# Optimization experiments

Measured on AMD Instinct MI355X. Metric: run time of the kernel, lower is better.

## Reference

```python
import jax, jax.numpy as jnp
import numpy as np

B, T, D, H, OUT_STEPS = 4096, 50, 64, 128, 100  # batch, warmup steps, latent dim, hidden units, rollout steps


def setup_inputs() -> dict:
    key = jax.random.key(0)
    ks = jax.random.split(key, 9)
    s = jnp.float32(0.05)  # keep gates out of saturation
    return {
        "x":   jax.random.normal(ks[0], (B, T, D), jnp.float32),
        "Wk0": jax.random.normal(ks[1], (D, 4 * H), jnp.float32) * s,
        "Wr0": jax.random.normal(ks[2], (H, 4 * H), jnp.float32) * s,
        "b0":  jax.random.normal(ks[3], (4 * H,), jnp.float32) * s,
        "Wk1": jax.random.normal(ks[4], (H, 4 * H), jnp.float32) * s,
        "Wr1": jax.random.normal(ks[5], (H, 4 * H), jnp.float32) * s,
        "b1":  jax.random.normal(ks[6], (4 * H,), jnp.float32) * s,
        "Wd":  jax.random.normal(ks[7], (H, D), jnp.float32) * s,
        "bd":  jax.random.normal(ks[8], (D,), jnp.float32) * s,
    }


def _lstm_cell(xt, h, c, Wk, Wr, b):
    # Keras LSTMCell: gates in order i, f, g(cell), o
    z = xt @ Wk + h @ Wr + b  # [B, 4H]
    i, f, g, o = jnp.split(z, 4, axis=-1)
    c_new = jax.nn.sigmoid(f) * c + jax.nn.sigmoid(i) * jnp.tanh(g)
    h_new = jax.nn.sigmoid(o) * jnp.tanh(c_new)
    return h_new, c_new


def reference(x, Wk0, Wr0, b0, Wk1, Wr1, b1, Wd, bd):
    Bn = x.shape[0]
    Hn = Wr0.shape[0]
    z = jnp.zeros((Bn, Hn), x.dtype)

    def warm_step(carry, xt):
        h0, c0, h1, c1 = carry
        h0, c0 = _lstm_cell(xt, h0, c0, Wk0, Wr0, b0)
        h1, c1 = _lstm_cell(h0, h1, c1, Wk1, Wr1, b1)
        return (h0, c0, h1, c1), None

    # warmup over the provided sequence (T >= min_warmup_steps=10)
    carry, _ = jax.lax.scan(warm_step, (z, z, z, z), jnp.swapaxes(x, 0, 1))
    pred0 = carry[2] @ Wd + bd  # Dense on last layer's hidden state

    def ar_step(carry, _):
        pred, h0, c0, h1, c1 = carry
        h0, c0 = _lstm_cell(pred, h0, c0, Wk0, Wr0, b0)
        h1, c1 = _lstm_cell(h0, h1, c1, Wk1, Wr1, b1)
        pred = h1 @ Wd + bd
        return (pred, h0, c0, h1, c1), pred

    _, preds = jax.lax.scan(ar_step, (pred0,) + carry, None, length=OUT_STEPS - 1)
    preds = jnp.concatenate([pred0[None], preds], axis=0)  # [OUT, B, D]
    return jnp.swapaxes(preds, 0, 1)  # [B, OUT, D]
```

## Files before the change

### kernel.cpp

```cpp
#include <hip/hip_runtime.h>
#include <hip/hip_bf16.h>

#define Tt   50
#define Dd   64
#define NOUT 100
#define G4   512
#define K0S  72
#define K1P  264
#define BM   16

typedef __attribute__((ext_vector_type(8))) short  short8;
typedef __attribute__((ext_vector_type(4))) float  floatx4;

#if __has_builtin(__builtin_amdgcn_exp2f)
#define EXP2(v) __builtin_amdgcn_exp2f(v)
#else
#define EXP2(v) exp2f(v)
#endif
__device__ __forceinline__ float rcp_(float v) { return __builtin_amdgcn_rcpf(v); }
#define KN2L2E (-2.8853900817779268f)

#define BARRIER() asm volatile("s_waitcnt lgkmcnt(0)\n\ts_barrier" ::: "memory")

__device__ __forceinline__ short f2bf(float f) {
    __hip_bfloat16 h = __float2bfloat16(f);
    return *reinterpret_cast<const short*>(&h);
}

#define W1F_OFF 196608
#define WDF_OFF 458752
#define B0F_OFF 475136
#define B1F_OFF 477184
#define BDF_OFF 479232

__global__ __launch_bounds__(256) void prep_kernel(
    const float* __restrict__ Wk0, const float* __restrict__ Wr0, const float* __restrict__ b0,
    const float* __restrict__ Wk1, const float* __restrict__ Wr1, const float* __restrict__ b1,
    const float* __restrict__ Wd,  const float* __restrict__ bd,  char* __restrict__ ws)
{
    int idx = blockIdx.x * 256 + threadIdx.x;
    short* w0f = (short*)ws;
    short* w1f = (short*)(ws + W1F_OFF);
    short* wdf = (short*)(ws + WDF_OFF);
    float* b0f = (float*)(ws + B0F_OFF);
    float* b1f = (float*)(ws + B1F_OFF);
    float* bdf = (float*)(ws + BDF_OFF);
    const float NL2E = -1.4426950408889634f;
    const float N2L2E = -2.8853900817779268f;

    if (idx < 98304) {
        int f = idx >> 9, r = idx & 511;
        int lane = r >> 3, j = r & 7;
        int nt = f / 6, kt = f - nt * 6;
        int k = kt * 32 + (lane >> 4) * 8 + j;
        int col = nt * 16 + (lane & 15);
        float sc = ((col >> 7) == 2) ? N2L2E : NL2E;
        w0f[idx] = f2bf(sc * ((k < Dd) ? Wk0[k * G4 + col] : Wr0[(k - Dd) * G4 + col]));
    } else if (idx < 229376) {
        int i2 = idx - 98304;
        int f = i2 >> 9, r = i2 & 511;
        int lane = r >> 3, j = r & 7;
        int nt = f >> 3, kt = f & 7;
        int k = kt * 32 + (lane >> 4) * 8 + j;
        int col = nt * 16 + (lane & 15);
        float sc = ((col >> 7) == 2) ? N2L2E : NL2E;
        w1f[i2] = f2bf(sc * ((k < 128) ? Wk1[k * G4 + col] : Wr1[(k - 128) * G4 + col]));
    } else if (idx < 237568) {
        int i2 = idx - 229376;
        int f = i2 >> 9, r = i2 & 511;
        int lane = r >> 3, j = r & 7;
        int nt = f >> 2, kt = f & 3;
        int k = kt * 32 + (lane >> 4) * 8 + j;
        int col = nt * 16 + (lane & 15);
        wdf[i2] = f2bf(Wd[k * Dd + col]);
    } else if (idx < 237568 + 1088) {
        int i2 = idx - 237568;
        if (i2 < 512) {
            float sc = ((i2 >> 7) == 2) ? N2L2E : NL2E;
            b0f[i2] = sc * b0[i2];
        } else if (i2 < 1024) {
            int c = i2 - 512;
            float sc = ((c >> 7) == 2) ? N2L2E : NL2E;
            b1f[c] = sc * b1[c];
        } else bdf[i2 - 1024] = bd[i2 - 1024];
    }
}

#define SM_A1  4608
#define SM_W0  21504
#define SM_TOT 152576
#define A0SZ   1152
#define A1SZ   4224

#define MFMA_B16(A, B, C) __builtin_amdgcn_mfma_f32_16x16x32_bf16((A), (B), (C), 0, 0, 0)

#define GATES(ACC, CS, BASE, COLOFF)                                                     \
    _Pragma("unroll")                                                                    \
    for (int rr = 0; rr < 4; ++rr) {                                                     \
        float Ei = EXP2(ACC[0][rr]);                                                     \
        float Ef = EXP2(ACC[1][rr]);                                                     \
        float Eg = EXP2(ACC[2][rr]);                                                     \
        float Eo = EXP2(ACC[3][rr]);                                                     \
        float ig = (1.0f - Eg) * rcp_((1.0f + Ei) * (1.0f + Eg));                        \
        float c_ = fmaf(rcp_(1.0f + Ef), CS[rr], ig);                                    \
        CS[rr] = c_;                                                                     \
        float Ec = EXP2(c_ * KN2L2E);                                                    \
        float h_ = (1.0f - Ec) * rcp_((1.0f + Eo) * (1.0f + Ec));                        \
        (BASE)[(quad * 4 + rr) * K1P + (COLOFF) + hu] = f2bf(h_);                        \
    }

#define ACC_INIT(ACC, B0_, B1_, B2_, B3_)            \
    ACC[0] = (floatx4){B0_, B0_, B0_, B0_};          \
    ACC[1] = (floatx4){B1_, B1_, B1_, B1_};          \
    ACC[2] = (floatx4){B2_, B2_, B2_, B2_};          \
    ACC[3] = (floatx4){B3_, B3_, B3_, B3_};

#define L0KT(KT)                                                                          \
    {                                                                                     \
        short8 af = ((KT) < 2)                                                            \
            ? *(const short8*)&a0p[l15 * K0S + (KT) * 32 + quad * 8]                      \
            : *(const short8*)&a1q[l15 * K1P + ((KT) - 2) * 32 + quad * 8];               \
        _Pragma("unroll")                                                                 \
        for (int g = 0; g < 4; ++g) {                                                     \
            const int pp = g * 6 + (KT);                                                  \
            short8 bfr = (pp < 16) ? *(const short8*)&w0l[((pp * 8 + w) << 9) + lane * 8] \
                                   : W0R[pp - 16];                                        \
            acc[g] = MFMA_B16(af, bfr, acc[g]);                                           \
        }                                                                                 \
    }

__global__ __launch_bounds__(512, 2) void lstm_kernel(
    const float* __restrict__ x, const char* __restrict__ ws, float* __restrict__ out)
{
    extern __shared__ char smem[];
    short* a0b = (short*)smem;
    short* a1b = (short*)(smem + SM_A1);
    short* w0l = (short*)(smem + SM_W0);

    const short* w0f = (const short*)ws;
    const short* w1f = (const short*)(ws + W1F_OFF);
    const short* wdf = (const short*)(ws + WDF_OFF);
    const float* b0f = (const float*)(ws + B0F_OFF);
    const float* b1f = (const float*)(ws + B1F_OFF);
    const float* bdf = (const float*)(ws + BDF_OFF);

    const int tid  = threadIdx.x;
    const int w    = tid >> 6;
    const int lane = tid & 63;
    const int l15  = lane & 15;
    const int quad = lane >> 4;
    const int row0 = blockIdx.x * BM;

    for (int i = tid; i < 2 * A0SZ; i += 512) a0b[i] = 0;
    for (int i = tid; i < 2 * A1SZ; i += 512) a1b[i] = 0;
    for (int c = tid; c < 8192; c += 512) {
        int e8 = c & 63;
        int wv = (c >> 6) & 7;
        int p  = c >> 9;
        int g = p / 6, kt = p - g * 6;
        const short* src = w0f + ((((g * 8 + wv) * 6) + kt) << 9) + e8 * 8;
        *(short8*)&w0l[((p * 8 + wv) << 9) + e8 * 8] = *(const short8*)src;
    }
    {
        int cx = tid & 63, rg2 = tid >> 6;
        a0b[rg2 * K0S + cx]       = f2bf(x[(size_t)(row0 + rg2) * (Tt * Dd) + cx]);
        a0b[(rg2 + 8) * K0S + cx] = f2bf(x[(size_t)(row0 + rg2 + 8) * (Tt * Dd) + cx]);
    }

    const short* w0rb = w0f + w * 3072 + lane * 8;
    const short* w1rb = w1f + w * 4096 + lane * 8;
    short8 W1R[4][8];
    #pragma unroll
    for (int g = 0; g < 4; ++g)
        #pragma unroll
        for (int kt = 0; kt < 8; ++kt)
            W1R[g][kt] = *(const short8*)(w1rb + g * 32768 + kt * 512);
    short8 W0R[8];
    #pragma unroll
    for (int p = 16; p < 24; ++p) {
        int g = p / 6, kt = p - g * 6;
        W0R[p - 16] = *(const short8*)(w0rb + g * 24576 + kt * 512);
    }
    short8 WdR[4];
    if (w < 4) {
        #pragma unroll
        for (int kt = 0; kt < 4; ++kt)
            WdR[kt] = *(const short8*)(wdf + ((w * 4 + kt) << 9) + lane * 8);
    }

    const int hu = w * 16 + l15;
    const float bi0 = b0f[hu], bff0 = b0f[128 + hu], bg0 = b0f[256 + hu], bo0 = b0f[384 + hu];
    const float bi1 = b1f[hu], bff1 = b1f[128 + hu], bg1 = b1f[256 + hu], bo1 = b1f[384 + hu];
    const float bdv = bdf[(w & 3) * 16 + l15];

    float c0s[4] = {0.f, 0.f, 0.f, 0.f};
    float c1s[4] = {0.f, 0.f, 0.f, 0.f};

    const int colx = tid & 63, rg = tid >> 6;

    __syncthreads();

    for (int step = 0; step < 149; ++step) {
        const int p = step & 1, q = p ^ 1;
        short* a0p = a0b + p * A0SZ;  short* a0q = a0b + q * A0SZ;
        short* a1p = a1b + p * A1SZ;  short* a1q = a1b + q * A1SZ;

        float xv0, xv1;
        if (step < Tt - 1) {
            xv0 = x[(size_t)(row0 + rg)     * (Tt * Dd) + (step + 1) * Dd + colx];
            xv1 = x[(size_t)(row0 + rg + 8) * (Tt * Dd) + (step + 1) * Dd + colx];
        }

        floatx4 acc[4];
        ACC_INIT(acc, bi0, bff0, bg0, bo0);
        __builtin_amdgcn_s_setprio(1);
        L0KT(2) L0KT(3) L0KT(4) L0KT(5) L0KT(0) L0KT(1)
        __builtin_amdgcn_s_setprio(0);

        GATES(acc, c0s, a1p, 0);

        if (step < Tt - 1) {
            a0q[rg * K0S + colx]       = f2bf(xv0);
            a0q[(rg + 8) * K0S + colx] = f2bf(xv1);
        }
        BARRIER();

        ACC_INIT(acc, bi1, bff1, bg1, bo1);
        __builtin_amdgcn_s_setprio(1);
        #pragma unroll
        for (int kt = 0; kt < 8; ++kt) {
            short8 af = *(const short8*)&a1p[l15 * K1P + kt * 32 + quad * 8];
            #pragma unroll
            for (int g = 0; g < 4; ++g)
                acc[g] = MFMA_B16(af, W1R[g][kt], acc[g]);
        }
        __builtin_amdgcn_s_setprio(0);

        GATES(acc, c1s, a1q, 128);

        if (step >= Tt - 1) {
            BARRIER();
            if (w < 4) {
                floatx4 ad0 = (floatx4){bdv, bdv, bdv, bdv};
                floatx4 ad1 = (floatx4){0.f, 0.f, 0.f, 0.f};
                __builtin_amdgcn_s_setprio(1);
                {
                    short8 a0_ = *(const short8*)&a1q[l15 * K1P + 128 +  0 + quad * 8];
                    short8 a1_ = *(const short8*)&a1q[l15 * K1P + 128 + 32 + quad * 8];
                    short8 a2_ = *(const short8*)&a1q[l15 * K1P + 128 + 64 + quad * 8];
                    short8 a3_ = *(const short8*)&a1q[l15 * K1P + 128 + 96 + quad * 8];
                    ad0 = MFMA_B16(a0_, WdR[0], ad0);
                    ad1 = MFMA_B16(a1_, WdR[1], ad1);
                    ad0 = MFMA_B16(a2_, WdR[2], ad0);
                    ad1 = MFMA_B16(a3_, WdR[3], ad1);
                }
                __builtin_amdgcn_s_setprio(0);
                float pv0 = ad0[0] + ad1[0], pv1 = ad0[1] + ad1[1];
                float pv2 = ad0[2] + ad1[2], pv3 = ad0[3] + ad1[3];
                int col = w * 16 + l15;
                a0q[(quad * 4 + 0) * K0S + col] = f2bf(pv0);
                a0q[(quad * 4 + 1) * K0S + col] = f2bf(pv1);
                a0q[(quad * 4 + 2) * K0S + col] = f2bf(pv2);
                a0q[(quad * 4 + 3) * K0S + col] = f2bf(pv3);
                int s = step - (Tt - 1);
                size_t ob = (size_t)(row0 + quad * 4) * (NOUT * Dd) + s * Dd + col;
                out[ob]                 = pv0;
                out[ob + 1 * NOUT * Dd] = pv1;
                out[ob + 2 * NOUT * Dd] = pv2;
                out[ob + 3 * NOUT * Dd] = pv3;
            }
            BARRIER();
        }
    }
}

extern "C" void kernel_launch(void* const* d_in, const int* in_sizes, int n_in,
                              void* d_out, int out_size, void* d_ws, size_t ws_size,
                              hipStream_t stream)
{
    (void)in_sizes; (void)n_in; (void)out_size; (void)ws_size;
    static_assert(SM_TOT <= 160 * 1024, "LDS budget");
    hipFuncSetAttribute(reinterpret_cast<const void*>(lstm_kernel),
                        hipFuncAttributeMaxDynamicSharedMemorySize, SM_TOT);
    prep_kernel<<<933, 256, 0, stream>>>(
        (const float*)d_in[1], (const float*)d_in[2], (const float*)d_in[3],
        (const float*)d_in[4], (const float*)d_in[5], (const float*)d_in[6],
        (const float*)d_in[7], (const float*)d_in[8], (char*)d_ws);
    lstm_kernel<<<256, 512, SM_TOT, stream>>>(
        (const float*)d_in[0], (const char*)d_ws, (float*)d_out);
}
```

Before: 468.6 us.

## Split warmup and rollout loops and overlap layer-1 recurrent MFMAs with barrier

Splits the single step loop into a warmup loop and an autoregressive loop, which removes the per-step branches on the step index. In the rollout loop, the layer-1 MFMAs over the h1 half of the input (k-tiles 4-7, written the previous step) are issued before the barrier. Only the k-tiles that depend on the freshly written h0 run after it. This shortens the critical path around the synchronisation in the sequential recurrence, in exchange for duplicated code and a larger instruction footprint.

```diff
diff --git a/kernel.cpp b/kernel.cpp
--- a/kernel.cpp
+++ b/kernel.cpp
@@ -129,6 +129,14 @@
         }                                                                                 \
     }
 
+#define L1KT(KT)                                                                          \
+    {                                                                                     \
+        short8 af = *(const short8*)&a1p[l15 * K1P + (KT) * 32 + quad * 8];               \
+        _Pragma("unroll")                                                                 \
+        for (int g = 0; g < 4; ++g)                                                       \
+            acc[g] = MFMA_B16(af, W1R[g][KT], acc[g]);                                    \
+    }
+
 __global__ __launch_bounds__(512, 2) void lstm_kernel(
     const float* __restrict__ x, const char* __restrict__ ws, float* __restrict__ out)
 {
@@ -200,16 +208,13 @@
 
     __syncthreads();
 
-    for (int step = 0; step < 149; ++step) {
+    for (int step = 0; step < 49; ++step) {
         const int p = step & 1, q = p ^ 1;
         short* a0p = a0b + p * A0SZ;  short* a0q = a0b + q * A0SZ;
         short* a1p = a1b + p * A1SZ;  short* a1q = a1b + q * A1SZ;
 
-        float xv0, xv1;
-        if (step < Tt - 1) {
-            xv0 = x[(size_t)(row0 + rg)     * (Tt * Dd) + (step + 1) * Dd + colx];
-            xv1 = x[(size_t)(row0 + rg + 8) * (Tt * Dd) + (step + 1) * Dd + colx];
-        }
+        float xv0 = x[(size_t)(row0 + rg)     * (Tt * Dd) + (step + 1) * Dd + colx];
+        float xv1 = x[(size_t)(row0 + rg + 8) * (Tt * Dd) + (step + 1) * Dd + colx];
 
         floatx4 acc[4];
         ACC_INIT(acc, bi0, bff0, bg0, bo0);
@@ -219,58 +224,77 @@
 
         GATES(acc, c0s, a1p, 0);
 
-        if (step < Tt - 1) {
-            a0q[rg * K0S + colx]       = f2bf(xv0);
-            a0q[(rg + 8) * K0S + colx] = f2bf(xv1);
+        a0q[rg * K0S + colx]       = f2bf(xv0);
+        a0q[(rg + 8) * K0S + colx] = f2bf(xv1);
+        BARRIER();
+
+        ACC_INIT(acc, bi1, bff1, bg1, bo1);
+        __builtin_amdgcn_s_setprio(1);
+        L1KT(0) L1KT(1) L1KT(2) L1KT(3) L1KT(4) L1KT(5) L1KT(6) L1KT(7)
+        __builtin_amdgcn_s_setprio(0);
+
+        GATES(acc, c1s, a1q, 128);
+    }
+
+    BARRIER();
+
+    for (int step = 49; step < 149; ++step) {
+        const int p = step & 1, q = p ^ 1;
+        short* a0p = a0b + p * A0SZ;  short* a0q = a0b + q * A0SZ;
+        short* a1p = a1b + p * A1SZ;  short* a1q = a1b + q * A1SZ;
+
+        floatx4 acc[4];
+        ACC_INIT(acc, bi0, bff0, bg0, bo0);
+        __builtin_amdgcn_s_setprio(1);
+        L0KT(2) L0KT(3) L0KT(4) L0KT(5) L0KT(0) L0KT(1)
+        __builtin_amdgcn_s_setprio(0);
+
+        GATES(acc, c0s, a1p, 0);
+
+        ACC_INIT(acc, bi1, bff1, bg1, bo1);
+        __builtin_amdgcn_s_setprio(1);
+        L1KT(4) L1KT(5) L1KT(6) L1KT(7)
+        __builtin_amdgcn_s_setprio(0);
+
+        BARRIER();
+
+        __builtin_amdgcn_s_setprio(1);
+        L1KT(0) L1KT(1) L1KT(2) L1KT(3)
+        __builtin_amdgcn_s_setprio(0);
+
+        GATES(acc, c1s, a1q, 128);
+
+        BARRIER();
+        if (w < 4) {
+            floatx4 ad0 = (floatx4){bdv, bdv, bdv, bdv};
+            floatx4 ad1 = (floatx4){0.f, 0.f, 0.f, 0.f};
+            __builtin_amdgcn_s_setprio(1);
+            {
+                short8 a0_ = *(const short8*)&a1q[l15 * K1P + 128 +  0 + quad * 8];
+                short8 a1_ = *(const short8*)&a1q[l15 * K1P + 128 + 32 + quad * 8];
+                short8 a2_ = *(const short8*)&a1q[l15 * K1P + 128 + 64 + quad * 8];
+                short8 a3_ = *(const short8*)&a1q[l15 * K1P + 128 + 96 + quad * 8];
+                ad0 = MFMA_B16(a0_, WdR[0], ad0);
+                ad1 = MFMA_B16(a1_, WdR[1], ad1);
+                ad0 = MFMA_B16(a2_, WdR[2], ad0);
+                ad1 = MFMA_B16(a3_, WdR[3], ad1);
+            }
+            __builtin_amdgcn_s_setprio(0);
+            float pv0 = ad0[0] + ad1[0], pv1 = ad0[1] + ad1[1];
+            float pv2 = ad0[2] + ad1[2], pv3 = ad0[3] + ad1[3];
+            int col = w * 16 + l15;
+            a0q[(quad * 4 + 0) * K0S + col] = f2bf(pv0);
+            a0q[(quad * 4 + 1) * K0S + col] = f2bf(pv1);
+            a0q[(quad * 4 + 2) * K0S + col] = f2bf(pv2);
+            a0q[(quad * 4 + 3) * K0S + col] = f2bf(pv3);
+            int s = step - (Tt - 1);
+            size_t ob = (size_t)(row0 + quad * 4) * (NOUT * Dd) + s * Dd + col;
+            out[ob]                 = pv0;
+            out[ob + 1 * NOUT * Dd] = pv1;
+            out[ob + 2 * NOUT * Dd] = pv2;
+            out[ob + 3 * NOUT * Dd] = pv3;
         }
         BARRIER();
-
-        ACC_INIT(acc, bi1, bff1, bg1, bo1);
-        __builtin_amdgcn_s_setprio(1);
-        #pragma unroll
-        for (int kt = 0; kt < 8; ++kt) {
-            short8 af = *(const short8*)&a1p[l15 * K1P + kt * 32 + quad * 8];
-            #pragma unroll
-            for (int g = 0; g < 4; ++g)
-                acc[g] = MFMA_B16(af, W1R[g][kt], acc[g]);
-        }
-        __builtin_amdgcn_s_setprio(0);
-
-        GATES(acc, c1s, a1q, 128);
-
-        if (step >= Tt - 1) {
-            BARRIER();
-            if (w < 4) {
-                floatx4 ad0 = (floatx4){bdv, bdv, bdv, bdv};
-                floatx4 ad1 = (floatx4){0.f, 0.f, 0.f, 0.f};
-                __builtin_amdgcn_s_setprio(1);
-                {
-                    short8 a0_ = *(const short8*)&a1q[l15 * K1P + 128 +  0 + quad * 8];
-                    short8 a1_ = *(const short8*)&a1q[l15 * K1P + 128 + 32 + quad * 8];
-                    short8 a2_ = *(const short8*)&a1q[l15 * K1P + 128 + 64 + quad * 8];
-                    short8 a3_ = *(const short8*)&a1q[l15 * K1P + 128 + 96 + quad * 8];
-                    ad0 = MFMA_B16(a0_, WdR[0], ad0);
-                    ad1 = MFMA_B16(a1_, WdR[1], ad1);
-                    ad0 = MFMA_B16(a2_, WdR[2], ad0);
-                    ad1 = MFMA_B16(a3_, WdR[3], ad1);
-                }
-                __builtin_amdgcn_s_setprio(0);
-                float pv0 = ad0[0] + ad1[0], pv1 = ad0[1] + ad1[1];
-                float pv2 = ad0[2] + ad1[2], pv3 = ad0[3] + ad1[3];
-                int col = w * 16 + l15;
-                a0q[(quad * 4 + 0) * K0S + col] = f2bf(pv0);
-                a0q[(quad * 4 + 1) * K0S + col] = f2bf(pv1);
-                a0q[(quad * 4 + 2) * K0S + col] = f2bf(pv2);
-                a0q[(quad * 4 + 3) * K0S + col] = f2bf(pv3);
-                int s = step - (Tt - 1);
-                size_t ob = (size_t)(row0 + quad * 4) * (NOUT * Dd) + s * Dd + col;
-                out[ob]                 = pv0;
-                out[ob + 1 * NOUT * Dd] = pv1;
-                out[ob + 2 * NOUT * Dd] = pv2;
-                out[ob + 3 * NOUT * Dd] = pv3;
-            }
-            BARRIER();
-        }
     }
 }
 
```

After: 475.2 us. About the same (+1.4%).
